# Kernel optimization log

Hardware: AMD Instinct MI355X
Metric: run time of the kernel (lower is better)

## Reference

```python
import jax, jax.numpy as jnp
import numpy as np

ALPHA = 0.2          # LeakyReLU negative slope
NEG_BIG = -9e15      # mask value from original code


def setup_inputs() -> dict:
    key = jax.random.key(0)
    k1, k2, k3, k4 = jax.random.split(key, 4)
    B, N, F_in, F_out = 16, 1024, 256, 256
    x = jax.random.normal(k1, (B, N, F_in), dtype=jnp.float32)
    adj = jax.random.randint(k2, (B, N, N), 0, 2, dtype=jnp.int32)
    # xavier-uniform-like scales
    W = jax.random.normal(k3, (F_in, F_out), dtype=jnp.float32) * np.sqrt(2.0 / (F_in + F_out))
    a = jax.random.normal(k4, (2 * F_out, 1), dtype=jnp.float32) * np.sqrt(2.0 / (2 * F_out + 1))
    return {"x": x, "adj": adj, "W": W, "a": a}


def reference(x, adj, W, a):
    # x: [B,N,Fin], adj: [B,N,N] (int mask), W: [Fin,Fout], a: [2*Fout,1]
    F_out = a.shape[0] // 2
    h = jnp.einsum("bni,io->bno", x, W)            # [B,N,Fout]
    # Decompose a into left/right halves: e_ij = lrelu(a_l.h_i + a_r.h_j)
    a_l = a[:F_out, 0]                               # [Fout]
    a_r = a[F_out:, 0]                               # [Fout]
    el = h @ a_l                                     # [B,N] score contribution of target i
    er = h @ a_r                                     # [B,N] score contribution of source j
    e = jax.nn.leaky_relu(el[:, :, None] + er[:, None, :], ALPHA)  # [B,N,N]
    e = jnp.where(adj > 0, e, NEG_BIG)
    attn = jax.nn.softmax(e, axis=-1)                # masked softmax over neighbors j
    # weighted sum of neighbor features; concat with n_heads=1 is identity
    return jnp.einsum("bij,bjo->bio", attn, h)       # [B,N,Fout]
```

## Files before the change

kernel.cpp:

```cpp
#include <hip/hip_runtime.h>
#include <stdint.h>

#define ALPHA 0.2f
#define NEG_BIG -9000000000000000.0f
#define L2E 1.4426950408889634f

typedef __attribute__((ext_vector_type(8))) short bf16x8;
typedef __attribute__((ext_vector_type(8))) unsigned short u16x8;
typedef __attribute__((ext_vector_type(4))) float f32x4;

__device__ __forceinline__ unsigned short f2bf(float f) {
    unsigned int u = __float_as_uint(f);
    u += 0x7fffu + ((u >> 16) & 1u);
    return (unsigned short)(u >> 16);
}

__device__ __forceinline__ void gload_lds16(const void* g, void* l) {
    __builtin_amdgcn_global_load_lds(
        (const __attribute__((address_space(1))) unsigned int*)g,
        (__attribute__((address_space(3))) unsigned int*)l, 16, 0, 0);
}

__global__ void wt_wa_kernel(const float* __restrict__ W,
                             const float* __restrict__ a,
                             unsigned short* __restrict__ Wtbf,
                             float* __restrict__ wa) {
    const int t = threadIdx.x;
    if (blockIdx.x < 256) {
        const int o = blockIdx.x;
        Wtbf[o * 256 + t] = f2bf(W[t * 256 + o]);
    } else {
        float sl = 0.f, sr = 0.f;
        const float* wr = W + t * 256;
        for (int o = 0; o < 256; ++o) {
            const float wv = wr[o];
            sl += wv * a[o];
            sr += wv * a[256 + o];
        }
        wa[t] = sl;
        wa[256 + t] = sr;
    }
}

__global__ __launch_bounds__(256) void eler2x_kernel(
    const float* __restrict__ x, const float* __restrict__ wa,
    float* __restrict__ el, float* __restrict__ er,
    unsigned short* __restrict__ xbf)
{
    const int w = threadIdx.x >> 6, l = threadIdx.x & 63;
    const int r = blockIdx.x * 4 + w;
    const float4 xv = *(const float4*)(x + (size_t)r * 256 + l * 4);
    const float4 al = *(const float4*)(wa + l * 4);
    const float4 ar = *(const float4*)(wa + 256 + l * 4);

    ushort4 xb;
    xb.x = f2bf(xv.x); xb.y = f2bf(xv.y); xb.z = f2bf(xv.z); xb.w = f2bf(xv.w);
    *(ushort4*)(xbf + (size_t)r * 256 + l * 4) = xb;

    float sl = xv.x * al.x + xv.y * al.y + xv.z * al.z + xv.w * al.w;
    float sr = xv.x * ar.x + xv.y * ar.y + xv.z * ar.z + xv.w * ar.w;
#pragma unroll
    for (int off = 32; off >= 1; off >>= 1) {
        sl += __shfl_xor(sl, off);
        sr += __shfl_xor(sr, off);
    }
    if (l == 0) { el[r] = sl * L2E; er[r] = sr * L2E; }
}

__global__ __launch_bounds__(256) void gemm_h(
    const unsigned short* __restrict__ A,
    const unsigned short* __restrict__ Bt,
    unsigned short* __restrict__ C)
{
    __shared__ __align__(16) unsigned short As[2 * 64 * 64];
    __shared__ __align__(16) unsigned short Bs[2 * 128 * 64];

    const int tid = threadIdx.x;
    const int w = tid >> 6, l = tid & 63;
    const int q = l >> 4, ml = l & 15;
    const int wm = (w >> 1) * 32;
    const int wn = (w & 1) * 64;
    const int m0 = blockIdx.y * 64;
    const int n0 = blockIdx.x * 128;

    f32x4 acc[2][4];
#pragma unroll
    for (int i = 0; i < 2; ++i)
#pragma unroll
        for (int j = 0; j < 4; ++j) {
            f32x4 z = {0.f, 0.f, 0.f, 0.f};
            acc[i][j] = z;
        }

#define GSTAGE(BI, K0) do {                                                   \
    _Pragma("unroll")                                                         \
    for (int c_ = 0; c_ < 2; ++c_) {                                          \
        const int cb_ = c_ * 256 + (w << 6);                                  \
        const int p_ = cb_ + l;                                               \
        const int r_ = p_ >> 3;                                               \
        const int cc_ = (p_ & 7) ^ (r_ & 7);                                  \
        gload_lds16(A + (size_t)(m0 + r_) * 256 + (K0) + cc_ * 8,             \
                    As + (BI) * 4096 + cb_ * 8);                              \
    }                                                                         \
    _Pragma("unroll")                                                         \
    for (int c_ = 0; c_ < 4; ++c_) {                                          \
        const int cb_ = c_ * 256 + (w << 6);                                  \
        const int p_ = cb_ + l;                                               \
        const int r_ = p_ >> 3;                                               \
        const int cc_ = (p_ & 7) ^ (r_ & 7);                                  \
        gload_lds16(Bt + (size_t)(n0 + r_) * 256 + (K0) + cc_ * 8,            \
                    Bs + (BI) * 8192 + cb_ * 8);                              \
    } } while (0)

    GSTAGE(0, 0);

    for (int s = 0; s < 4; ++s) {
        const int cur = s & 1;
        if (s + 1 < 4) {
            GSTAGE((s + 1) & 1, (s + 1) * 64);
            asm volatile("s_waitcnt vmcnt(6) lgkmcnt(0)" ::: "memory");
        } else {
            asm volatile("s_waitcnt vmcnt(0) lgkmcnt(0)" ::: "memory");
        }
        __builtin_amdgcn_s_barrier();
        __builtin_amdgcn_sched_barrier(0);

        const unsigned short* Ab = As + cur * 4096;
        const unsigned short* Bb = Bs + cur * 8192;
        bf16x8 aF[2][2], bF[2][4];
#pragma unroll
        for (int ks = 0; ks < 2; ++ks) {
#pragma unroll
            for (int mt = 0; mt < 2; ++mt) {
                const int mm = wm + mt * 16 + ml;
                aF[ks][mt] = *(const bf16x8*)(Ab + (mm * 8 + ((ks * 4 + q) ^ (mm & 7))) * 8);
            }
#pragma unroll
            for (int nt = 0; nt < 4; ++nt) {
                const int nn = wn + nt * 16 + ml;
                bF[ks][nt] = *(const bf16x8*)(Bb + (nn * 8 + ((ks * 4 + q) ^ (nn & 7))) * 8);
            }
        }
#pragma unroll
        for (int ks = 0; ks < 2; ++ks)
            for (int mt = 0; mt < 2; ++mt)
                for (int nt = 0; nt < 4; ++nt)
                    acc[mt][nt] = __builtin_amdgcn_mfma_f32_16x16x32_bf16(
                        aF[ks][mt], bF[ks][nt], acc[mt][nt], 0, 0, 0);

        asm volatile("s_waitcnt lgkmcnt(0)" ::: "memory");
        __builtin_amdgcn_s_barrier();
    }
#undef GSTAGE

    for (int mt = 0; mt < 2; ++mt)
        for (int nt = 0; nt < 4; ++nt) {
            const int gn = n0 + wn + nt * 16 + ml;
            for (int r = 0; r < 4; ++r) {
                const int gm = m0 + wm + mt * 16 + q * 4 + r;
                C[(size_t)gm * 16384 + gn] = f2bf(acc[mt][nt][r]);
            }
        }
}

__global__ __launch_bounds__(512) void maskpv_kernel(
    const int* __restrict__ adj,
    const float* __restrict__ el2,
    const float* __restrict__ er2,
    const unsigned short* __restrict__ hT,
    float* __restrict__ out)
{
    __shared__ float er_s[1024];
    __shared__ float c_s[64];
    __shared__ __align__(16) unsigned short Hs[2 * 256 * 32];
    __shared__ __align__(16) unsigned short Ps[2 * 64 * 40];

    const int tid = threadIdx.x;
    const int w = tid >> 6, l = tid & 63;
    const int q = l >> 4, ml = l & 15;
    const int wm = (w >> 2) * 32;
    const int wn = (w & 3) * 64;

    const int bid = blockIdx.x;
    const int slot = bid >> 3;
    const int b = ((bid & 7) << 1) | (slot >> 4);
    const int i0 = (slot & 15) * 64;

    const int ib = tid >> 3;
    const int js = (tid & 7) * 4;
    const int rg = (b << 10) + i0 + ib;
    const float el2i = el2[rg];

    const unsigned short* hb = hT + (size_t)b * 1024;

#define STAGE(BI, T) do {                                                     \
    const int jb_ = (T) * 32;                                                 \
    _Pragma("unroll")                                                         \
    for (int c_ = 0; c_ < 2; ++c_) {                                          \
        const int cb_ = c_ * 512 + tid;                                       \
        const int r_ = cb_ >> 2;                                              \
        const int cc_ = (cb_ & 3) ^ ((r_ >> 1) & 3);                          \
        gload_lds16(hb + (size_t)r_ * 16384 + jb_ + cc_ * 8,                  \
                    Hs + (BI) * 8192 + (cb_ << 3));                           \
    } } while (0)

    STAGE(0, 0);

    *(float2*)(er_s + tid * 2) = *(const float2*)(er2 + (b << 10) + tid * 2);
    asm volatile("s_waitcnt lgkmcnt(0)" ::: "memory");
    __builtin_amdgcn_s_barrier();

    unsigned mw[4];
    float m1 = -3.0e38f, s1 = 0.f;
    const int* arow = adj + (size_t)rg * 1024 + js;
#pragma unroll
    for (int kw = 0; kw < 4; ++kw) {
        unsigned wbits = 0;
#pragma unroll
        for (int j = 0; j < 8; ++j) {
            const int k = kw * 8 + j;
            const int4 av = *(const int4*)(arow + k * 32);
            const float4 erv = *(const float4*)(er_s + js + k * 32);
            float e0 = el2i + erv.x; e0 = fmaxf(e0, ALPHA * e0);
            float e1 = el2i + erv.y; e1 = fmaxf(e1, ALPHA * e1);
            float e2 = el2i + erv.z; e2 = fmaxf(e2, ALPHA * e2);
            float e3 = el2i + erv.w; e3 = fmaxf(e3, ALPHA * e3);
            e0 = av.x > 0 ? e0 : -3.0e38f;
            e1 = av.y > 0 ? e1 : -3.0e38f;
            e2 = av.z > 0 ? e2 : -3.0e38f;
            e3 = av.w > 0 ? e3 : -3.0e38f;
            wbits |= ((av.x > 0 ? 1u : 0u) | (av.y > 0 ? 2u : 0u) |
                      (av.z > 0 ? 4u : 0u) | (av.w > 0 ? 8u : 0u)) << (j * 4);
            const float mc = fmaxf(fmaxf(e0, e1), fmaxf(e2, e3));
            const float nm = fmaxf(m1, mc);
            s1 = s1 * exp2f(m1 - nm) + exp2f(e0 - nm) + exp2f(e1 - nm)
               + exp2f(e2 - nm) + exp2f(e3 - nm);
            m1 = nm;
        }
        mw[kw] = wbits;
    }
#pragma unroll
    for (int off = 1; off <= 4; off <<= 1) {
        const float mo = __shfl_xor(m1, off);
        const float so = __shfl_xor(s1, off);
        const float nm = fmaxf(m1, mo);
        s1 = s1 * exp2f(m1 - nm) + so * exp2f(mo - nm);
        m1 = nm;
    }
    if ((tid & 7) == 0) c_s[ib] = m1 + log2f(s1);
    asm volatile("s_waitcnt lgkmcnt(0)" ::: "memory");
    __builtin_amdgcn_s_barrier();
    const float c2i = c_s[ib];

    f32x4 acc[2][4];
#pragma unroll
    for (int i = 0; i < 2; ++i)
#pragma unroll
        for (int j = 0; j < 4; ++j) {
            f32x4 z = {0.f, 0.f, 0.f, 0.f};
            acc[i][j] = z;
        }

#define BUILDR(BI, T) do {                                                    \
    const int jb_ = (T) * 32;                                                 \
    const float4 ev_ = *(const float4*)(er_s + jb_ + js);                     \
    const unsigned mv_ = (mw[(T) >> 3] >> (((T) & 7) * 4)) & 0xFu;            \
    float e0_ = el2i + ev_.x; e0_ = fmaxf(e0_, ALPHA * e0_);                  \
    float e1_ = el2i + ev_.y; e1_ = fmaxf(e1_, ALPHA * e1_);                  \
    float e2_ = el2i + ev_.z; e2_ = fmaxf(e2_, ALPHA * e2_);                  \
    float e3_ = el2i + ev_.w; e3_ = fmaxf(e3_, ALPHA * e3_);                  \
    ushort4 pv_;                                                              \
    pv_.x = (mv_ & 1u) ? f2bf(exp2f(e0_ - c2i)) : (unsigned short)0;          \
    pv_.y = (mv_ & 2u) ? f2bf(exp2f(e1_ - c2i)) : (unsigned short)0;          \
    pv_.z = (mv_ & 4u) ? f2bf(exp2f(e2_ - c2i)) : (unsigned short)0;          \
    pv_.w = (mv_ & 8u) ? f2bf(exp2f(e3_ - c2i)) : (unsigned short)0;          \
    *(ushort4*)(Ps + (BI) * 2560 + ib * 40 + js) = pv_;                       \
    } while (0)

#define COMPUTE(BI) do {                                                      \
    bf16x8 aF_[2], bF_[4];                                                    \
    _Pragma("unroll")                                                         \
    for (int mt_ = 0; mt_ < 2; ++mt_)                                         \
        aF_[mt_] = *(const bf16x8*)(Ps + (BI) * 2560 +                        \
                                    (wm + mt_ * 16 + ml) * 40 + q * 8);       \
    _Pragma("unroll")                                                         \
    for (int nt_ = 0; nt_ < 4; ++nt_) {                                       \
        const int oc_ = wn + nt_ * 16 + ml;                                   \
        const int sl_ = q ^ ((oc_ >> 1) & 3);                                 \
        bF_[nt_] = *(const bf16x8*)(Hs + (BI) * 8192 + oc_ * 32 + sl_ * 8);   \
    }                                                                         \
    _Pragma("unroll")                                                         \
    for (int mt_ = 0; mt_ < 2; ++mt_)                                         \
        _Pragma("unroll")                                                     \
        for (int nt_ = 0; nt_ < 4; ++nt_)                                     \
            acc[mt_][nt_] = __builtin_amdgcn_mfma_f32_16x16x32_bf16(          \
                aF_[mt_], bF_[nt_], acc[mt_][nt_], 0, 0, 0);                  \
    } while (0)

#pragma unroll
    for (int t = 0; t < 32; ++t) {
        const int cur = t & 1;
        if (t + 1 < 32) STAGE((t + 1) & 1, t + 1);
        BUILDR(cur, t);
        if (t + 1 < 32)
            asm volatile("s_waitcnt vmcnt(2) lgkmcnt(0)" ::: "memory");
        else
            asm volatile("s_waitcnt vmcnt(0) lgkmcnt(0)" ::: "memory");
        __builtin_amdgcn_s_barrier();
        __builtin_amdgcn_sched_barrier(0);
        COMPUTE(cur);
        asm volatile("s_waitcnt lgkmcnt(0)" ::: "memory");
        __builtin_amdgcn_s_barrier();
    }

#undef STAGE
#undef BUILDR
#undef COMPUTE

    float* ob = out + (size_t)b * 262144;
#pragma unroll
    for (int mt = 0; mt < 2; ++mt)
#pragma unroll
        for (int nt = 0; nt < 4; ++nt) {
            const int gn = wn + nt * 16 + ml;
#pragma unroll
            for (int r = 0; r < 4; ++r) {
                const int gm = i0 + wm + mt * 16 + q * 4 + r;
                ob[(size_t)gm * 256 + gn] = acc[mt][nt][r];
            }
        }
}

extern "C" void kernel_launch(void* const* d_in, const int* in_sizes, int n_in,
                              void* d_out, int out_size, void* d_ws, size_t ws_size,
                              hipStream_t stream) {
    const float* x   = (const float*)d_in[0];
    const int*   adj = (const int*)d_in[1];
    const float* W   = (const float*)d_in[2];
    const float* a   = (const float*)d_in[3];
    float* out = (float*)d_out;

    char* ws = (char*)d_ws;
    unsigned short* Wtbf  = (unsigned short*)(ws);
    float* wa             = (float*)(ws + 131072);
    unsigned short* xbf   = (unsigned short*)(ws + 133120);
    unsigned short* h_T   = (unsigned short*)(ws + 8521728);
    float* el             = (float*)(ws + 16910336);
    float* er             = (float*)(ws + 16975872);

    wt_wa_kernel<<<dim3(257), dim3(256), 0, stream>>>(W, a, Wtbf, wa);

    eler2x_kernel<<<dim3(4096), dim3(256), 0, stream>>>(x, wa, el, er, xbf);

    gemm_h<<<dim3(128, 4), dim3(256), 0, stream>>>(Wtbf, xbf, h_T);

    maskpv_kernel<<<dim3(256), dim3(512), 0, stream>>>(adj, el, er, h_T, out);
}
```

Measured before the change: 169.6 us.

## Halve row tile to 32 rows, double K step to 64, two-pass softmax stats

Each workgroup of the masked attention-times-H kernel now handles 32 query rows instead of 64, so the grid grows to 512 workgroups. Each pipeline step now covers 64 source columns instead of 32, with a wider XOR swizzle on the staged H tile. The online max/sum softmax statistics are replaced by a max pass followed by a sum pass with four accumulators, which removes the rescaling exp2 calls. This fills more compute units and halves the loop iteration and barrier count. In exchange, each H^T slice is reloaded by twice as many workgroups, and the doubled H buffer uses more LDS per workgroup.

Result: faster. 153.5 us (-9.5%).

```diff
diff --git a/kernel.cpp b/kernel.cpp
--- a/kernel.cpp
+++ b/kernel.cpp
@@ -171,37 +171,37 @@
     float* __restrict__ out)
 {
     __shared__ float er_s[1024];
-    __shared__ float c_s[64];
-    __shared__ __align__(16) unsigned short Hs[2 * 256 * 32];
-    __shared__ __align__(16) unsigned short Ps[2 * 64 * 40];
+    __shared__ float c_s[32];
+    __shared__ __align__(16) unsigned short Hs[2 * 256 * 64];
+    __shared__ __align__(16) unsigned short Ps[2 * 32 * 72];
 
     const int tid = threadIdx.x;
     const int w = tid >> 6, l = tid & 63;
     const int q = l >> 4, ml = l & 15;
-    const int wm = (w >> 2) * 32;
+    const int wm = (w >> 2) * 16;
     const int wn = (w & 3) * 64;
 
     const int bid = blockIdx.x;
     const int slot = bid >> 3;
-    const int b = ((bid & 7) << 1) | (slot >> 4);
-    const int i0 = (slot & 15) * 64;
-
-    const int ib = tid >> 3;
-    const int js = (tid & 7) * 4;
+    const int b = ((bid & 7) << 1) | (slot >> 5);
+    const int i0 = (slot & 31) * 32;
+
+    const int ib = tid >> 4;
+    const int js = (tid & 15) * 4;
     const int rg = (b << 10) + i0 + ib;
     const float el2i = el2[rg];
 
     const unsigned short* hb = hT + (size_t)b * 1024;
 
 #define STAGE(BI, T) do {                                                     \
-    const int jb_ = (T) * 32;                                                 \
-    _Pragma("unroll")                                                         \
-    for (int c_ = 0; c_ < 2; ++c_) {                                          \
+    const int jb_ = (T) * 64;                                                 \
+    _Pragma("unroll")                                                         \
+    for (int c_ = 0; c_ < 4; ++c_) {                                          \
         const int cb_ = c_ * 512 + tid;                                       \
-        const int r_ = cb_ >> 2;                                              \
-        const int cc_ = (cb_ & 3) ^ ((r_ >> 1) & 3);                          \
+        const int r_ = cb_ >> 3;                                              \
+        const int cc_ = (cb_ & 7) ^ (r_ & 7);                                 \
         gload_lds16(hb + (size_t)r_ * 16384 + jb_ + cc_ * 8,                  \
-                    Hs + (BI) * 8192 + (cb_ << 3));                           \
+                    Hs + (BI) * 16384 + (cb_ << 3));                          \
     } } while (0)
 
     STAGE(0, 0);
@@ -210,61 +210,62 @@
     asm volatile("s_waitcnt lgkmcnt(0)" ::: "memory");
     __builtin_amdgcn_s_barrier();
 
-    unsigned mw[4];
-    float m1 = -3.0e38f, s1 = 0.f;
+    unsigned mw0 = 0, mw1 = 0;
+    float m1 = -3.0e38f;
     const int* arow = adj + (size_t)rg * 1024 + js;
 #pragma unroll
-    for (int kw = 0; kw < 4; ++kw) {
-        unsigned wbits = 0;
-#pragma unroll
-        for (int j = 0; j < 8; ++j) {
-            const int k = kw * 8 + j;
-            const int4 av = *(const int4*)(arow + k * 32);
-            const float4 erv = *(const float4*)(er_s + js + k * 32);
-            float e0 = el2i + erv.x; e0 = fmaxf(e0, ALPHA * e0);
-            float e1 = el2i + erv.y; e1 = fmaxf(e1, ALPHA * e1);
-            float e2 = el2i + erv.z; e2 = fmaxf(e2, ALPHA * e2);
-            float e3 = el2i + erv.w; e3 = fmaxf(e3, ALPHA * e3);
-            e0 = av.x > 0 ? e0 : -3.0e38f;
-            e1 = av.y > 0 ? e1 : -3.0e38f;
-            e2 = av.z > 0 ? e2 : -3.0e38f;
-            e3 = av.w > 0 ? e3 : -3.0e38f;
-            wbits |= ((av.x > 0 ? 1u : 0u) | (av.y > 0 ? 2u : 0u) |
-                      (av.z > 0 ? 4u : 0u) | (av.w > 0 ? 8u : 0u)) << (j * 4);
-            const float mc = fmaxf(fmaxf(e0, e1), fmaxf(e2, e3));
-            const float nm = fmaxf(m1, mc);
-            s1 = s1 * exp2f(m1 - nm) + exp2f(e0 - nm) + exp2f(e1 - nm)
-               + exp2f(e2 - nm) + exp2f(e3 - nm);
-            m1 = nm;
-        }
-        mw[kw] = wbits;
-    }
-#pragma unroll
-    for (int off = 1; off <= 4; off <<= 1) {
-        const float mo = __shfl_xor(m1, off);
-        const float so = __shfl_xor(s1, off);
-        const float nm = fmaxf(m1, mo);
-        s1 = s1 * exp2f(m1 - nm) + so * exp2f(mo - nm);
-        m1 = nm;
-    }
-    if ((tid & 7) == 0) c_s[ib] = m1 + log2f(s1);
+    for (int k = 0; k < 16; ++k) {
+        const int4 av = *(const int4*)(arow + k * 64);
+        const float4 erv = *(const float4*)(er_s + k * 64 + js);
+        float e0 = el2i + erv.x; e0 = fmaxf(e0, ALPHA * e0);
+        float e1 = el2i + erv.y; e1 = fmaxf(e1, ALPHA * e1);
+        float e2 = el2i + erv.z; e2 = fmaxf(e2, ALPHA * e2);
+        float e3 = el2i + erv.w; e3 = fmaxf(e3, ALPHA * e3);
+        const unsigned bits = (av.x > 0 ? 1u : 0u) | (av.y > 0 ? 2u : 0u) |
+                              (av.z > 0 ? 4u : 0u) | (av.w > 0 ? 8u : 0u);
+        e0 = av.x > 0 ? e0 : -3.0e38f;
+        e1 = av.y > 0 ? e1 : -3.0e38f;
+        e2 = av.z > 0 ? e2 : -3.0e38f;
+        e3 = av.w > 0 ? e3 : -3.0e38f;
+        m1 = fmaxf(m1, fmaxf(fmaxf(e0, e1), fmaxf(e2, e3)));
+        if (k < 8) mw0 |= bits << (k * 4); else mw1 |= bits << ((k - 8) * 4);
+    }
+#pragma unroll
+    for (int off = 1; off <= 8; off <<= 1) m1 = fmaxf(m1, __shfl_xor(m1, off));
+
+    float s0 = 0.f, s1 = 0.f, s2 = 0.f, s3 = 0.f;
+#pragma unroll
+    for (int k = 0; k < 16; ++k) {
+        const float4 erv = *(const float4*)(er_s + k * 64 + js);
+        const unsigned mv = ((k < 8) ? (mw0 >> (k * 4)) : (mw1 >> ((k - 8) * 4))) & 0xFu;
+        float e0 = el2i + erv.x; e0 = fmaxf(e0, ALPHA * e0);
+        float e1 = el2i + erv.y; e1 = fmaxf(e1, ALPHA * e1);
+        float e2 = el2i + erv.z; e2 = fmaxf(e2, ALPHA * e2);
+        float e3 = el2i + erv.w; e3 = fmaxf(e3, ALPHA * e3);
+        s0 += (mv & 1u) ? exp2f(e0 - m1) : 0.f;
+        s1 += (mv & 2u) ? exp2f(e1 - m1) : 0.f;
+        s2 += (mv & 4u) ? exp2f(e2 - m1) : 0.f;
+        s3 += (mv & 8u) ? exp2f(e3 - m1) : 0.f;
+    }
+    float ssum = (s0 + s1) + (s2 + s3);
+#pragma unroll
+    for (int off = 1; off <= 8; off <<= 1) ssum += __shfl_xor(ssum, off);
+    if ((tid & 15) == 0) c_s[ib] = m1 + log2f(ssum);
     asm volatile("s_waitcnt lgkmcnt(0)" ::: "memory");
     __builtin_amdgcn_s_barrier();
     const float c2i = c_s[ib];
 
-    f32x4 acc[2][4];
-#pragma unroll
-    for (int i = 0; i < 2; ++i)
-#pragma unroll
-        for (int j = 0; j < 4; ++j) {
-            f32x4 z = {0.f, 0.f, 0.f, 0.f};
-            acc[i][j] = z;
-        }
+    f32x4 acc[4];
+#pragma unroll
+    for (int j = 0; j < 4; ++j) {
+        f32x4 z = {0.f, 0.f, 0.f, 0.f};
+        acc[j] = z;
+    }
 
 #define BUILDR(BI, T) do {                                                    \
-    const int jb_ = (T) * 32;                                                 \
-    const float4 ev_ = *(const float4*)(er_s + jb_ + js);                     \
-    const unsigned mv_ = (mw[(T) >> 3] >> (((T) & 7) * 4)) & 0xFu;            \
+    const float4 ev_ = *(const float4*)(er_s + (T) * 64 + js);                \
+    const unsigned mv_ =                                                      \
+        (((T) < 8) ? (mw0 >> ((T) * 4)) : (mw1 >> (((T) - 8) * 4))) & 0xFu;   \
     float e0_ = el2i + ev_.x; e0_ = fmaxf(e0_, ALPHA * e0_);                  \
     float e1_ = el2i + ev_.y; e1_ = fmaxf(e1_, ALPHA * e1_);                  \
     float e2_ = el2i + ev_.z; e2_ = fmaxf(e2_, ALPHA * e2_);                  \
@@ -274,36 +275,39 @@
     pv_.y = (mv_ & 2u) ? f2bf(exp2f(e1_ - c2i)) : (unsigned short)0;          \
     pv_.z = (mv_ & 4u) ? f2bf(exp2f(e2_ - c2i)) : (unsigned short)0;          \
     pv_.w = (mv_ & 8u) ? f2bf(exp2f(e3_ - c2i)) : (unsigned short)0;          \
-    *(ushort4*)(Ps + (BI) * 2560 + ib * 40 + js) = pv_;                       \
+    *(ushort4*)(Ps + (BI) * 2304 + ib * 72 + js) = pv_;                       \
     } while (0)
 
 #define COMPUTE(BI) do {                                                      \
-    bf16x8 aF_[2], bF_[4];                                                    \
-    _Pragma("unroll")                                                         \
-    for (int mt_ = 0; mt_ < 2; ++mt_)                                         \
-        aF_[mt_] = *(const bf16x8*)(Ps + (BI) * 2560 +                        \
-                                    (wm + mt_ * 16 + ml) * 40 + q * 8);       \
-    _Pragma("unroll")                                                         \
-    for (int nt_ = 0; nt_ < 4; ++nt_) {                                       \
-        const int oc_ = wn + nt_ * 16 + ml;                                   \
-        const int sl_ = q ^ ((oc_ >> 1) & 3);                                 \
-        bF_[nt_] = *(const bf16x8*)(Hs + (BI) * 8192 + oc_ * 32 + sl_ * 8);   \
-    }                                                                         \
-    _Pragma("unroll")                                                         \
-    for (int mt_ = 0; mt_ < 2; ++mt_)                                         \
+    bf16x8 aF_[2], bF_[2][4];                                                 \
+    _Pragma("unroll")                                                         \
+    for (int ks_ = 0; ks_ < 2; ++ks_)                                         \
+        aF_[ks_] = *(const bf16x8*)(Ps + (BI) * 2304 +                        \
+                                    (wm + ml) * 72 + ks_ * 32 + q * 8);       \
+    _Pragma("unroll")                                                         \
+    for (int ks_ = 0; ks_ < 2; ++ks_)                                         \
+        _Pragma("unroll")                                                     \
+        for (int nt_ = 0; nt_ < 4; ++nt_) {                                   \
+            const int oc_ = wn + nt_ * 16 + ml;                               \
+            const int sl_ = (ks_ * 4 + q) ^ (oc_ & 7);                        \
+            bF_[ks_][nt_] = *(const bf16x8*)(Hs + (BI) * 16384 +              \
+                                             oc_ * 64 + sl_ * 8);             \
+        }                                                                     \
+    _Pragma("unroll")                                                         \
+    for (int ks_ = 0; ks_ < 2; ++ks_)                                         \
         _Pragma("unroll")                                                     \
         for (int nt_ = 0; nt_ < 4; ++nt_)                                     \
-            acc[mt_][nt_] = __builtin_amdgcn_mfma_f32_16x16x32_bf16(          \
-                aF_[mt_], bF_[nt_], acc[mt_][nt_], 0, 0, 0);                  \
+            acc[nt_] = __builtin_amdgcn_mfma_f32_16x16x32_bf16(               \
+                aF_[ks_], bF_[ks_][nt_], acc[nt_], 0, 0, 0);                  \
     } while (0)
 
 #pragma unroll
-    for (int t = 0; t < 32; ++t) {
+    for (int t = 0; t < 16; ++t) {
         const int cur = t & 1;
-        if (t + 1 < 32) STAGE((t + 1) & 1, t + 1);
+        if (t + 1 < 16) STAGE((t + 1) & 1, t + 1);
         BUILDR(cur, t);
-        if (t + 1 < 32)
-            asm volatile("s_waitcnt vmcnt(2) lgkmcnt(0)" ::: "memory");
+        if (t + 1 < 16)
+            asm volatile("s_waitcnt vmcnt(4) lgkmcnt(0)" ::: "memory");
         else
             asm volatile("s_waitcnt vmcnt(0) lgkmcnt(0)" ::: "memory");
         __builtin_amdgcn_s_barrier();
@@ -319,16 +323,14 @@
 
     float* ob = out + (size_t)b * 262144;
 #pragma unroll
-    for (int mt = 0; mt < 2; ++mt)
-#pragma unroll
-        for (int nt = 0; nt < 4; ++nt) {
-            const int gn = wn + nt * 16 + ml;
-#pragma unroll
-            for (int r = 0; r < 4; ++r) {
-                const int gm = i0 + wm + mt * 16 + q * 4 + r;
-                ob[(size_t)gm * 256 + gn] = acc[mt][nt][r];
-            }
-        }
+    for (int nt = 0; nt < 4; ++nt) {
+        const int gn = wn + nt * 16 + ml;
+#pragma unroll
+        for (int r = 0; r < 4; ++r) {
+            const int gm = i0 + wm + q * 4 + r;
+            ob[(size_t)gm * 256 + gn] = acc[nt][r];
+        }
+    }
 }
 
 extern "C" void kernel_launch(void* const* d_in, const int* in_sizes, int n_in,
@@ -354,5 +356,5 @@
 
     gemm_h<<<dim3(128, 4), dim3(256), 0, stream>>>(Wtbf, xbf, h_T);
 
-    maskpv_kernel<<<dim3(256), dim3(512), 0, stream>>>(adj, el, er, h_T, out);
-}
+    maskpv_kernel<<<dim3(512), dim3(512), 0, stream>>>(adj, el, er, h_T, out);
+}
```
